# Performance work log

Measured on AMD Instinct MI355X. Metric: run time of the kernel, lower is better.

The kernel has to match this reference:

```python
import jax, jax.numpy as jnp
import numpy as np

B, L, D, H = 2, 2048, 1024, 16
DH = D // H  # dim_head = 64
NEG_INF = 1e12


def setup_inputs() -> dict:
    key = jax.random.key(0)
    ks = jax.random.split(key, 12)
    s_in = 1.0 / np.sqrt(D)
    inp = {
        "q": jax.random.normal(ks[0], (B, L, D), jnp.float32),
        "k": jax.random.normal(ks[1], (B, L, D), jnp.float32),
        "v": jax.random.normal(ks[2], (B, L, D), jnp.float32),
        # causal mask, True = position is masked (matches masked_fill_ semantics)
        "mask": jnp.broadcast_to(
            jnp.triu(jnp.ones((L, L), jnp.bool_), k=1)[None, None], (B, 1, L, L)
        ),
        # torch Linear weight is [out, in]; store transposed [in, out] for x @ W
        "Wq": jax.random.normal(ks[3], (D, D), jnp.float32) * s_in,
        "bq": jnp.zeros((D,), jnp.float32),
        "Wk": jax.random.normal(ks[4], (D, D), jnp.float32) * s_in,
        "bk": jnp.zeros((D,), jnp.float32),
        "Wv": jax.random.normal(ks[5], (D, D), jnp.float32) * s_in,
        "bv": jnp.zeros((D,), jnp.float32),
        "Wo": jax.random.normal(ks[6], (D, D), jnp.float32) * s_in,
        "bo": jnp.zeros((D,), jnp.float32),
    }
    return inp


def _split_heads(x):
    # [b, l, h*d] -> [b, h, l, d]
    b, l, _ = x.shape
    return x.reshape(b, l, H, DH).transpose(0, 2, 1, 3)


def reference(q, k, v, mask, Wq, bq, Wk, bk, Wv, bv, Wo, bo):
    Q = _split_heads(q @ Wq + bq)
    K = _split_heads(k @ Wk + bk)
    V = _split_heads(v @ Wv + bv)
    scale = 1.0 / np.sqrt(DH)
    dots = jnp.einsum("bhqd,bhkd->bhqk", Q, K) * scale  # [b, h, L, L]
    dots = jnp.where(mask, -NEG_INF, dots)
    attn = jax.nn.softmax(dots, axis=-1)
    out = jnp.einsum("bhqk,bhkd->bhqd", attn, V)  # [b, h, L, d]
    out = out.transpose(0, 2, 1, 3).reshape(q.shape[0], q.shape[1], D)
    return out @ Wo + bo
```

## Files before the change

### kernel.cpp

```cpp
#include <hip/hip_runtime.h>
#include <stdint.h>

typedef __bf16 bf16;
typedef bf16 bf16x8 __attribute__((ext_vector_type(8)));
typedef bf16 bf16x4 __attribute__((ext_vector_type(4)));
typedef float f32x4 __attribute__((ext_vector_type(4)));

constexpr int B_ = 2, L_ = 2048, D_ = 1024, H_ = 16, DH_ = 64;
constexpr int M_ = B_ * L_;
constexpr float QSCALE = 0.125f * 1.44269504f;

__device__ __forceinline__ void gload_lds16(const void* g, void* l) {
  __builtin_amdgcn_global_load_lds(
      (const __attribute__((address_space(1))) unsigned int*)g,
      (__attribute__((address_space(3))) unsigned int*)l, 16, 0, 0);
}
#define MEMBAR() asm volatile("" ::: "memory")
__device__ __forceinline__ void block_bar() {
  MEMBAR(); __builtin_amdgcn_s_barrier(); MEMBAR();
}

__global__ void cast3(const float* __restrict__ q, const float* __restrict__ k,
                      const float* __restrict__ v, bf16* __restrict__ dst) {
  const float* src = blockIdx.y == 0 ? q : (blockIdx.y == 1 ? k : v);
  size_t i = (size_t)blockIdx.x * blockDim.x + threadIdx.x;
  float4 val = reinterpret_cast<const float4*>(src)[i];
  bf16x4 o;
  o[0] = (bf16)val.x; o[1] = (bf16)val.y; o[2] = (bf16)val.z; o[3] = (bf16)val.w;
  reinterpret_cast<bf16x4*>(dst + (size_t)blockIdx.y * M_ * D_)[i] = o;
}

__global__ void transpose_cast_w(const float* __restrict__ W0, const float* __restrict__ W1,
                                 const float* __restrict__ W2, const float* __restrict__ W3,
                                 bf16* __restrict__ WT) {
  __shared__ float tile[32][33];
  const float* W = blockIdx.z == 0 ? W0 : blockIdx.z == 1 ? W1 : blockIdx.z == 2 ? W2 : W3;
  bf16* Wt = WT + (size_t)blockIdx.z * D_ * D_;
  int tx = threadIdx.x, ty = threadIdx.y;
  int r0 = blockIdx.y * 32, c0 = blockIdx.x * 32;
#pragma unroll
  for (int i = 0; i < 32; i += 8)
    tile[ty + i][tx] = W[(size_t)(r0 + ty + i) * D_ + c0 + tx];
  __syncthreads();
#pragma unroll
  for (int i = 0; i < 32; i += 8)
    Wt[(size_t)(c0 + ty + i) * D_ + r0 + tx] = (bf16)tile[tx][ty + i];
}

constexpr int BM = 128, BN = 64, BK = 64;

template <int MODE>
__global__ __launch_bounds__(256) void gemm_bf16(
    const bf16* __restrict__ A, const bf16* __restrict__ Bt,
    const float* __restrict__ bias, void* __restrict__ outp, float oscale) {
  __shared__ bf16 As[2][BM * BK];
  __shared__ bf16 Bs[2][BN * BK];
  const int tid = threadIdx.x;
  const int wid = tid >> 6, lane = tid & 63;
  const int lr = lane & 15, lg = lane >> 4;
  const int wr = wid >> 1, wc = wid & 1;

  const int bidf = blockIdx.y * gridDim.x + blockIdx.x;
  const int cpx = (gridDim.x * gridDim.y) >> 3;
  const int swz = (bidf & 7) * cpx + (bidf >> 3);
  const int n0 = (swz % gridDim.x) * BN, m0 = (swz / gridDim.x) * BM;

  f32x4 acc[4][2] = {};

  auto stage = [&](int bsel, int kt) {
#pragma unroll
    for (int i = 0; i < 4; ++i) {
      int slot = i * 4 + wid;
      int c = slot * 64 + lane;
      int row = c >> 3, cs = c & 7, g = cs ^ (row & 7);
      gload_lds16(A + (size_t)(m0 + row) * D_ + kt + g * 8, (char*)As[bsel] + slot * 1024);
    }
#pragma unroll
    for (int i = 0; i < 2; ++i) {
      int slot = i * 4 + wid;
      int c = slot * 64 + lane;
      int row = c >> 3, cs = c & 7, g = cs ^ (row & 7);
      gload_lds16(Bt + (size_t)(n0 + row) * D_ + kt + g * 8, (char*)Bs[bsel] + slot * 1024);
    }
  };

  stage(0, 0);
  for (int t = 0; t < D_ / BK; ++t) {
    const int cur = t & 1;
    if (t < D_ / BK - 1) {
      stage(cur ^ 1, (t + 1) * BK);
      asm volatile("s_waitcnt vmcnt(6)" ::: "memory");
    } else {
      asm volatile("s_waitcnt vmcnt(0)" ::: "memory");
    }
    block_bar();
#pragma unroll
    for (int kk = 0; kk < 2; ++kk) {
      bf16x8 af[4], bfr[2];
#pragma unroll
      for (int i = 0; i < 4; ++i) {
        int R = wr * 64 + i * 16 + lr;
        int ch = (kk * 4 + lg) ^ (R & 7);
        af[i] = *(const bf16x8*)((char*)As[cur] + R * 128 + ch * 16);
      }
#pragma unroll
      for (int j = 0; j < 2; ++j) {
        int R = wc * 32 + j * 16 + lr;
        int ch = (kk * 4 + lg) ^ (R & 7);
        bfr[j] = *(const bf16x8*)((char*)Bs[cur] + R * 128 + ch * 16);
      }
#pragma unroll
      for (int i = 0; i < 4; ++i)
#pragma unroll
        for (int j = 0; j < 2; ++j)
          acc[i][j] = __builtin_amdgcn_mfma_f32_16x16x32_bf16(af[i], bfr[j], acc[i][j], 0, 0, 0);
    }
    block_bar();
  }

#pragma unroll
  for (int i = 0; i < 4; ++i) {
#pragma unroll
    for (int j = 0; j < 2; ++j) {
      const int n = n0 + wc * 32 + j * 16 + lr;
      const float bn = bias[n];
      const int mbase = m0 + wr * 64 + i * 16 + lg * 4;
      if constexpr (MODE == 2) {
        float* out = (float*)outp;
#pragma unroll
        for (int r = 0; r < 4; ++r)
          out[(size_t)(mbase + r) * D_ + n] = acc[i][j][r] + bn;
      } else if constexpr (MODE == 0) {
        bf16* out = (bf16*)outp;
        const int h = n >> 6, dh = n & 63;
#pragma unroll
        for (int r = 0; r < 4; ++r) {
          int m = mbase + r;
          int b = m >> 11, l = m & (L_ - 1);
          out[((size_t)(b * H_ + h) * L_ + l) * DH_ + dh] = (bf16)((acc[i][j][r] + bn) * oscale);
        }
      } else {
        bf16* out = (bf16*)outp;
        const int h = n >> 6, dh = n & 63;
        int b = mbase >> 11, l = mbase & (L_ - 1);
        bf16x4 pk;
#pragma unroll
        for (int r = 0; r < 4; ++r) pk[r] = (bf16)(acc[i][j][r] + bn);
        *(bf16x4*)(out + ((size_t)(b * H_ + h) * DH_ + dh) * L_ + l) = pk;
      }
    }
  }
}

__global__ __launch_bounds__(128, 2) void attn_fwd(
    const bf16* __restrict__ Q,
    const bf16* __restrict__ K,
    const bf16* __restrict__ Vt,
    bf16* __restrict__ O) {
  __shared__ bf16 Ks[2][64 * 64];
  __shared__ bf16 Vs[2][64 * 64];
  __shared__ bf16 Ps[2][16 * 72];
  const int tid = threadIdx.x;
  const int wid = tid >> 6, lane = tid & 63;
  const int lr = lane & 15, lg = lane >> 4;
  const int x = blockIdx.x;
  const int h = blockIdx.y, b = blockIdx.z;
  const size_t bh = (size_t)b * H_ + h;
  const int qtA = x, qtB = 63 - x;
  const int qr0A = qtA * 32 + wid * 16, qr0B = qtB * 32 + wid * 16;
  const int ktmaxA = (qtA * 32 + 31) >> 6, ktmaxB = (qtB * 32 + 31) >> 6;

  bf16x8 qfA[2], qfB[2];
  {
    const bf16* qa = Q + (bh * L_ + qr0A) * DH_;
    const bf16* qb = Q + (bh * L_ + qr0B) * DH_;
#pragma unroll
    for (int kk = 0; kk < 2; ++kk) {
      qfA[kk] = *(const bf16x8*)(qa + lr * DH_ + kk * 32 + lg * 8);
      qfB[kk] = *(const bf16x8*)(qb + lr * DH_ + kk * 32 + lg * 8);
    }
  }

  f32x4 oA[4] = {}, oB[4] = {};
  float mA[4], lA[4], mB[4], lB[4];
#pragma unroll
  for (int r = 0; r < 4; ++r) { mA[r] = mB[r] = -3.0e38f; lA[r] = lB[r] = 0.f; }

  auto stage = [&](int bsel, int kt) {
    const bf16* kb = K + (bh * L_ + (size_t)kt * 64) * DH_;
    const bf16* vb = Vt + bh * (size_t)DH_ * L_ + (size_t)kt * 64;
#pragma unroll
    for (int i = 0; i < 4; ++i) {
      int slot = i * 2 + wid;
      int c = slot * 64 + lane;
      int row = c >> 3, cs = c & 7, g = cs ^ (row & 7);
      gload_lds16(kb + (size_t)row * DH_ + g * 8, (char*)Ks[bsel] + slot * 1024);
      gload_lds16(vb + (size_t)row * L_ + g * 8, (char*)Vs[bsel] + slot * 1024);
    }
  };

  bf16* pw = &Ps[wid][0];

  auto smx_pv = [&](f32x4* s, float* m, float* l, f32x4* o, int cur) {
    float t[4];
#pragma unroll
    for (int r = 0; r < 4; ++r)
      t[r] = fmaxf(fmaxf(s[0][r], s[1][r]), fmaxf(s[2][r], s[3][r]));
#pragma unroll
    for (int d = 1; d < 16; d <<= 1)
#pragma unroll
      for (int r = 0; r < 4; ++r) t[r] = fmaxf(t[r], __shfl_xor(t[r], d));
    bool need = false;
#pragma unroll
    for (int r = 0; r < 4; ++r) need |= (t[r] > m[r] + 11.0f);
    if (__any(need)) {
#pragma unroll
      for (int r = 0; r < 4; ++r) {
        float mn = fmaxf(m[r], t[r]);
        float c = exp2f(m[r] - mn);
        m[r] = mn; l[r] *= c;
#pragma unroll
        for (int j = 0; j < 4; ++j) o[j][r] *= c;
      }
    }
    float rs[4] = {0.f, 0.f, 0.f, 0.f};
#pragma unroll
    for (int j = 0; j < 4; ++j)
#pragma unroll
      for (int r = 0; r < 4; ++r) {
        float p = exp2f(s[j][r] - m[r]);
        s[j][r] = p;
        rs[r] += p;
      }
#pragma unroll
    for (int d = 1; d < 16; d <<= 1)
#pragma unroll
      for (int r = 0; r < 4; ++r) rs[r] += __shfl_xor(rs[r], d);
#pragma unroll
    for (int r = 0; r < 4; ++r) l[r] += rs[r];
#pragma unroll
    for (int j = 0; j < 4; ++j)
#pragma unroll
      for (int r = 0; r < 4; ++r)
        pw[(lg * 4 + r) * 72 + j * 16 + lr] = (bf16)s[j][r];
    bf16x8 ap[2];
#pragma unroll
    for (int st = 0; st < 2; ++st)
      ap[st] = *(const bf16x8*)(pw + lr * 72 + st * 32 + lg * 8);
#pragma unroll
    for (int j = 0; j < 4; ++j)
#pragma unroll
      for (int st = 0; st < 2; ++st) {
        int dh = j * 16 + lr;
        int ch = (st * 4 + lg) ^ (dh & 7);
        bf16x8 bv = *(const bf16x8*)((char*)Vs[cur] + dh * 128 + ch * 16);
        o[j] = __builtin_amdgcn_mfma_f32_16x16x32_bf16(ap[st], bv, o[j], 0, 0, 0);
      }
  };

  stage(0, 0);
  for (int kt = 0; kt <= ktmaxB; ++kt) {
    const int cur = kt & 1;
    if (kt < ktmaxB) {
      stage(cur ^ 1, kt + 1);
      asm volatile("s_waitcnt vmcnt(8)" ::: "memory");
    } else {
      asm volatile("s_waitcnt vmcnt(0)" ::: "memory");
    }
    block_bar();
    const bool actA = (kt <= ktmaxA);

    f32x4 sB[4] = {}, sA[4] = {};
#pragma unroll
    for (int kk = 0; kk < 2; ++kk)
#pragma unroll
      for (int j = 0; j < 4; ++j) {
        int key = j * 16 + lr;
        int ch = (kk * 4 + lg) ^ (key & 7);
        bf16x8 bk = *(const bf16x8*)((char*)Ks[cur] + key * 128 + ch * 16);
        sB[j] = __builtin_amdgcn_mfma_f32_16x16x32_bf16(qfB[kk], bk, sB[j], 0, 0, 0);
        if (actA) sA[j] = __builtin_amdgcn_mfma_f32_16x16x32_bf16(qfA[kk], bk, sA[j], 0, 0, 0);
      }

    if (kt == ktmaxB) {
#pragma unroll
      for (int j = 0; j < 4; ++j) {
        int key = kt * 64 + j * 16 + lr;
#pragma unroll
        for (int r = 0; r < 4; ++r)
          if (key > qr0B + lg * 4 + r) sB[j][r] = -1.0e30f;
      }
    }
    if (actA && kt == ktmaxA) {
#pragma unroll
      for (int j = 0; j < 4; ++j) {
        int key = kt * 64 + j * 16 + lr;
#pragma unroll
        for (int r = 0; r < 4; ++r)
          if (key > qr0A + lg * 4 + r) sA[j][r] = -1.0e30f;
      }
    }

    smx_pv(sB, mB, lB, oB, cur);
    if (actA) smx_pv(sA, mA, lA, oA, cur);
    block_bar();
  }

#pragma unroll
  for (int j = 0; j < 4; ++j)
#pragma unroll
    for (int r = 0; r < 4; ++r) {
      int dh = j * 16 + lr;
      O[((size_t)b * L_ + qr0A + lg * 4 + r) * D_ + h * DH_ + dh] = (bf16)(oA[j][r] / lA[r]);
      O[((size_t)b * L_ + qr0B + lg * 4 + r) * D_ + h * DH_ + dh] = (bf16)(oB[j][r] / lB[r]);
    }
}

extern "C" void kernel_launch(void* const* d_in, const int* in_sizes, int n_in,
                              void* d_out, int out_size, void* d_ws, size_t ws_size,
                              hipStream_t stream) {
  const float* q  = (const float*)d_in[0];
  const float* k  = (const float*)d_in[1];
  const float* v  = (const float*)d_in[2];
  const float* Wq = (const float*)d_in[4];
  const float* bq = (const float*)d_in[5];
  const float* Wk = (const float*)d_in[6];
  const float* bk = (const float*)d_in[7];
  const float* Wv = (const float*)d_in[8];
  const float* bv = (const float*)d_in[9];
  const float* Wo = (const float*)d_in[10];
  const float* bo = (const float*)d_in[11];

  char* ws = (char*)d_ws;
  bf16* castQ = (bf16*)ws;
  bf16* castK = (bf16*)(ws + (8ull << 20));
  bf16* castV = (bf16*)(ws + (16ull << 20));
  bf16* WT    = (bf16*)(ws + (24ull << 20));
  bf16* Vtb   = (bf16*)(ws + (32ull << 20));
  bf16* Kb    = (bf16*)(ws + (16ull << 20));
  bf16* Qb    = (bf16*)(ws + (8ull << 20));
  bf16* Ob    = (bf16*)ws;

  transpose_cast_w<<<dim3(32, 32, 4), dim3(32, 8), 0, stream>>>(Wq, Wk, Wv, Wo, WT);
  cast3<<<dim3((M_ * D_ / 4) / 256, 3), 256, 0, stream>>>(q, k, v, castQ);

  dim3 gg(D_ / BN, M_ / BM);
  gemm_bf16<1><<<gg, 256, 0, stream>>>(castV, WT + 2ull * D_ * D_, bv, Vtb, 1.0f);
  gemm_bf16<0><<<gg, 256, 0, stream>>>(castK, WT + 1ull * D_ * D_, bk, Kb, 1.0f);
  gemm_bf16<0><<<gg, 256, 0, stream>>>(castQ, WT, bq, Qb, QSCALE);

  attn_fwd<<<dim3(32, H_, B_), 128, 0, stream>>>(Qb, Kb, Vtb, Ob);

  gemm_bf16<2><<<gg, 256, 0, stream>>>(Ob, WT + 3ull * D_ * D_, bo, (float*)d_out, 1.0f);
}
```

Baseline: 286.3 us.

## Load K and V fragments directly from global memory instead of LDS staging

Removes the double-buffered LDS staging of K and V tiles, which used async global-to-LDS loads, and has each wave read its MFMA operands straight from global memory into registers. This frees LDS, which may allow more occupancy, and removes the staging copies and waitcnt logic. In exchange, both waves now load the same K/V data redundantly, the loads are strided global accesses with no prefetch overlap, and latency is exposed directly before the MFMAs.

```diff
diff --git a/kernel.cpp b/kernel.cpp
--- a/kernel.cpp
+++ b/kernel.cpp
@@ -157,8 +157,6 @@
     const bf16* __restrict__ K,
     const bf16* __restrict__ Vt,
     bf16* __restrict__ O) {
-  __shared__ bf16 Ks[2][64 * 64];
-  __shared__ bf16 Vs[2][64 * 64];
   __shared__ bf16 Ps[2][16 * 72];
   const int tid = threadIdx.x;
   const int wid = tid >> 6, lane = tid & 63;
@@ -186,37 +184,24 @@
 #pragma unroll
   for (int r = 0; r < 4; ++r) { mA[r] = mB[r] = -3.0e38f; lA[r] = lB[r] = 0.f; }
 
-  auto stage = [&](int bsel, int kt) {
-    const bf16* kb = K + (bh * L_ + (size_t)kt * 64) * DH_;
-    const bf16* vb = Vt + bh * (size_t)DH_ * L_ + (size_t)kt * 64;
-#pragma unroll
-    for (int i = 0; i < 4; ++i) {
-      int slot = i * 2 + wid;
-      int c = slot * 64 + lane;
-      int row = c >> 3, cs = c & 7, g = cs ^ (row & 7);
-      gload_lds16(kb + (size_t)row * DH_ + g * 8, (char*)Ks[bsel] + slot * 1024);
-      gload_lds16(vb + (size_t)row * L_ + g * 8, (char*)Vs[bsel] + slot * 1024);
-    }
-  };
-
   bf16* pw = &Ps[wid][0];
 
-  auto smx_pv = [&](f32x4* s, float* m, float* l, f32x4* o, int cur) {
-    float t[4];
+  auto smx_pv = [&](f32x4* s, float* m, float* l, f32x4* o, const bf16* vb) {
+    float t4[4];
 #pragma unroll
     for (int r = 0; r < 4; ++r)
-      t[r] = fmaxf(fmaxf(s[0][r], s[1][r]), fmaxf(s[2][r], s[3][r]));
+      t4[r] = fmaxf(fmaxf(s[0][r], s[1][r]), fmaxf(s[2][r], s[3][r]));
 #pragma unroll
     for (int d = 1; d < 16; d <<= 1)
 #pragma unroll
-      for (int r = 0; r < 4; ++r) t[r] = fmaxf(t[r], __shfl_xor(t[r], d));
+      for (int r = 0; r < 4; ++r) t4[r] = fmaxf(t4[r], __shfl_xor(t4[r], d));
     bool need = false;
 #pragma unroll
-    for (int r = 0; r < 4; ++r) need |= (t[r] > m[r] + 11.0f);
+    for (int r = 0; r < 4; ++r) need |= (t4[r] > m[r] + 11.0f);
     if (__any(need)) {
 #pragma unroll
       for (int r = 0; r < 4; ++r) {
-        float mn = fmaxf(m[r], t[r]);
+        float mn = fmaxf(m[r], t4[r]);
         float c = exp2f(m[r] - mn);
         m[r] = mn; l[r] *= c;
 #pragma unroll
@@ -248,39 +233,34 @@
     for (int st = 0; st < 2; ++st)
       ap[st] = *(const bf16x8*)(pw + lr * 72 + st * 32 + lg * 8);
 #pragma unroll
-    for (int j = 0; j < 4; ++j)
-#pragma unroll
-      for (int st = 0; st < 2; ++st) {
-        int dh = j * 16 + lr;
-        int ch = (st * 4 + lg) ^ (dh & 7);
-        bf16x8 bv = *(const bf16x8*)((char*)Vs[cur] + dh * 128 + ch * 16);
-        o[j] = __builtin_amdgcn_mfma_f32_16x16x32_bf16(ap[st], bv, o[j], 0, 0, 0);
-      }
+    for (int j = 0; j < 4; ++j) {
+      const bf16* vr = vb + (size_t)(j * 16 + lr) * L_ + lg * 8;
+      bf16x8 v0 = *(const bf16x8*)vr;
+      bf16x8 v1 = *(const bf16x8*)(vr + 32);
+      o[j] = __builtin_amdgcn_mfma_f32_16x16x32_bf16(ap[0], v0, o[j], 0, 0, 0);
+      o[j] = __builtin_amdgcn_mfma_f32_16x16x32_bf16(ap[1], v1, o[j], 0, 0, 0);
+    }
   };
 
-  stage(0, 0);
   for (int kt = 0; kt <= ktmaxB; ++kt) {
-    const int cur = kt & 1;
-    if (kt < ktmaxB) {
-      stage(cur ^ 1, kt + 1);
-      asm volatile("s_waitcnt vmcnt(8)" ::: "memory");
-    } else {
-      asm volatile("s_waitcnt vmcnt(0)" ::: "memory");
-    }
     block_bar();
     const bool actA = (kt <= ktmaxA);
-
-    f32x4 sB[4] = {}, sA[4] = {};
-#pragma unroll
-    for (int kk = 0; kk < 2; ++kk)
-#pragma unroll
-      for (int j = 0; j < 4; ++j) {
-        int key = j * 16 + lr;
-        int ch = (kk * 4 + lg) ^ (key & 7);
-        bf16x8 bk = *(const bf16x8*)((char*)Ks[cur] + key * 128 + ch * 16);
-        sB[j] = __builtin_amdgcn_mfma_f32_16x16x32_bf16(qfB[kk], bk, sB[j], 0, 0, 0);
-        if (actA) sA[j] = __builtin_amdgcn_mfma_f32_16x16x32_bf16(qfA[kk], bk, sA[j], 0, 0, 0);
-      }
+    const bf16* kb = K + (bh * L_ + (size_t)kt * 64) * DH_;
+    const bf16* vb = Vt + bh * (size_t)DH_ * L_ + (size_t)kt * 64;
+
+    f32x4 sA[4] = {}, sB[4] = {};
+#pragma unroll
+    for (int j = 0; j < 4; ++j) {
+      const bf16* kr = kb + (size_t)(j * 16 + lr) * DH_ + lg * 8;
+      bf16x8 k0 = *(const bf16x8*)kr;
+      bf16x8 k1 = *(const bf16x8*)(kr + 32);
+      sB[j] = __builtin_amdgcn_mfma_f32_16x16x32_bf16(qfB[0], k0, sB[j], 0, 0, 0);
+      sB[j] = __builtin_amdgcn_mfma_f32_16x16x32_bf16(qfB[1], k1, sB[j], 0, 0, 0);
+      if (actA) {
+        sA[j] = __builtin_amdgcn_mfma_f32_16x16x32_bf16(qfA[0], k0, sA[j], 0, 0, 0);
+        sA[j] = __builtin_amdgcn_mfma_f32_16x16x32_bf16(qfA[1], k1, sA[j], 0, 0, 0);
+      }
+    }
 
     if (kt == ktmaxB) {
 #pragma unroll
@@ -291,18 +271,19 @@
           if (key > qr0B + lg * 4 + r) sB[j][r] = -1.0e30f;
       }
     }
-    if (actA && kt == ktmaxA) {
-#pragma unroll
-      for (int j = 0; j < 4; ++j) {
-        int key = kt * 64 + j * 16 + lr;
-#pragma unroll
-        for (int r = 0; r < 4; ++r)
-          if (key > qr0A + lg * 4 + r) sA[j][r] = -1.0e30f;
-      }
-    }
-
-    smx_pv(sB, mB, lB, oB, cur);
-    if (actA) smx_pv(sA, mA, lA, oA, cur);
+    smx_pv(sB, mB, lB, oB, vb);
+    if (actA) {
+      if (kt == ktmaxA) {
+#pragma unroll
+        for (int j = 0; j < 4; ++j) {
+          int key = kt * 64 + j * 16 + lr;
+#pragma unroll
+          for (int r = 0; r < 4; ++r)
+            if (key > qr0A + lg * 4 + r) sA[j][r] = -1.0e30f;
+        }
+      }
+      smx_pv(sA, mA, lA, oA, vb);
+    }
     block_bar();
   }
 
```

Result: slower. 326.7 us (+14.1%).
